# Optimization experiments

Hardware: AMD Instinct MI355X
Metric: run time of the kernel (lower is better)

The kernel has to match this reference:

```python
import jax, jax.numpy as jnp
import numpy as np

B, T, E, H = 4, 2048, 1024, 16
HS = E // H  # head_size = 64
FFN_HID = 100  # hard-coded in FeedForward
EPS = 1e-5


def layernorm(x, g, b):
    mu = jnp.mean(x, axis=-1, keepdims=True)
    var = jnp.mean(jnp.square(x - mu), axis=-1, keepdims=True)
    return (x - mu) * jax.lax.rsqrt(var + EPS) * g + b


def setup_inputs() -> dict:
    key = jax.random.key(0)
    ks = jax.random.split(key, 10)
    s = E ** -0.5
    return {
        "x": jax.random.normal(ks[0], (B, T, E), jnp.float32),
        "wq": jax.random.normal(ks[1], (E, E), jnp.float32) * s,
        "wk": jax.random.normal(ks[2], (E, E), jnp.float32) * s,
        "wv": jax.random.normal(ks[3], (E, E), jnp.float32) * s,
        "w_proj": jax.random.normal(ks[4], (E, E), jnp.float32) * s,
        "b_proj": jnp.zeros((E,), jnp.float32),
        "w1": jax.random.normal(ks[5], (E, FFN_HID), jnp.float32) * s,
        "b1": jnp.zeros((FFN_HID,), jnp.float32),
        "w2": jax.random.normal(ks[6], (FFN_HID, E), jnp.float32) * (FFN_HID ** -0.5),
        "b2": jnp.zeros((E,), jnp.float32),
        "ln1_g": jnp.ones((E,), jnp.float32),
        "ln1_b": jnp.zeros((E,), jnp.float32),
        "ln2_g": jnp.ones((E,), jnp.float32),
        "ln2_b": jnp.zeros((E,), jnp.float32),
    }


def reference(x, wq, wk, wv, w_proj, b_proj, w1, b1, w2, b2, ln1_g, ln1_b, ln2_g, ln2_b):
    # --- self-attention with pre-LN residual ---
    h = layernorm(x, ln1_g, ln1_b)  # [B,T,E]
    def split_heads(y):  # [B,T,E] -> [B,H,T,HS]
        return y.reshape(B, T, H, HS).transpose(0, 2, 1, 3)
    q = split_heads(h @ wq)
    k = split_heads(h @ wk)
    v = split_heads(h @ wv)
    # NOTE: original scales by C**-0.5 with C = n_embd (not head_size)
    wei = jnp.einsum("bhtd,bhsd->bhts", q, k) * (E ** -0.5)  # [B,H,T,T]
    causal = jnp.tril(jnp.ones((T, T), bool))
    wei = jnp.where(causal, wei, -jnp.inf)
    wei = jax.nn.softmax(wei, axis=-1)
    att = jnp.einsum("bhts,bhsd->bhtd", wei, v)  # [B,H,T,HS]
    att = att.transpose(0, 2, 1, 3).reshape(B, T, E)  # concat heads
    x = x + att @ w_proj + b_proj
    # --- feedforward with pre-LN residual ---
    h2 = layernorm(x, ln2_g, ln2_b)
    ff = jax.nn.relu(h2 @ w1 + b1) @ w2 + b2
    return x + ff
```

## Files before the change

### kernel.cpp

```cpp
#include <hip/hip_runtime.h>

typedef unsigned short u16;
typedef unsigned int u32;
typedef __bf16 bf16x8 __attribute__((ext_vector_type(8)));
typedef float f32x4 __attribute__((ext_vector_type(4)));

#define BDIM 4
#define TDIM 2048
#define EDIM 1024
#define HDIM 16
#define HS 64
#define MROWS (BDIM * TDIM)
#define FFNP 128

__device__ __forceinline__ u16 f2bf(float f) {
    __bf16 h = (__bf16)f;
    return __builtin_bit_cast(u16, h);
}

__device__ __forceinline__ void glds16(const void* g, void* l) {
    __builtin_amdgcn_global_load_lds(
        (__attribute__((address_space(1))) const void*)g,
        (__attribute__((address_space(3))) void*)l, 16, 0, 0);
}

__global__ __launch_bounds__(256) void transpose_all(
    const float* __restrict__ wq, const float* __restrict__ wk,
    const float* __restrict__ wv, const float* __restrict__ wproj,
    const float* __restrict__ w1, const float* __restrict__ w2,
    u16* __restrict__ wqkvt, u16* __restrict__ wpt,
    u16* __restrict__ w1t, u16* __restrict__ w2t)
{
    __shared__ u16 sm[64][72];
    const float* src; u16* dst;
    int K, N, Kpad, Npad;
    switch (blockIdx.z) {
        case 0: src = wq;    dst = wqkvt;                 K = N = Kpad = Npad = 1024; break;
        case 1: src = wk;    dst = wqkvt + 1024 * 1024;   K = N = Kpad = Npad = 1024; break;
        case 2: src = wv;    dst = wqkvt + 2 * 1024 * 1024; K = N = Kpad = Npad = 1024; break;
        case 3: src = wproj; dst = wpt;                   K = N = Kpad = Npad = 1024; break;
        case 4: src = w1;    dst = w1t; K = 1024; N = 100; Kpad = 1024; Npad = 128; break;
        default: src = w2;   dst = w2t; K = 100; N = 1024; Kpad = 128; Npad = 1024; break;
    }
    int k0 = blockIdx.x * 64, n0 = blockIdx.y * 64;
    if (k0 >= Kpad || n0 >= Npad) return;
    int tid = threadIdx.x;
#pragma unroll
    for (int i = 0; i < 16; i++) {
        int idx = i * 256 + tid;
        int kl = idx >> 6, nl = idx & 63;
        int k = k0 + kl, n = n0 + nl;
        float v = (k < K && n < N) ? src[(size_t)k * N + n] : 0.f;
        sm[kl][nl] = f2bf(v);
    }
    __syncthreads();
#pragma unroll
    for (int i = 0; i < 16; i++) {
        int idx = i * 256 + tid;
        int nl = idx >> 6, kl = idx & 63;
        int n = n0 + nl, k = k0 + kl;
        if (n < Npad && k < Kpad) dst[(size_t)n * Kpad + k] = sm[kl][nl];
    }
}

__global__ __launch_bounds__(256) void ln_rows(
    const float* __restrict__ X, const float* __restrict__ G,
    const float* __restrict__ Bv, u16* __restrict__ H)
{
    int w = threadIdx.x >> 6, l = threadIdx.x & 63;
    int row = blockIdx.x * 4 + w;
    const float* xr = X + (size_t)row * EDIM;
    float4 v[4];
    float s = 0.f, s2 = 0.f;
#pragma unroll
    for (int i = 0; i < 4; i++) {
        v[i] = *(const float4*)&xr[l * 4 + i * 256];
        s += v[i].x + v[i].y + v[i].z + v[i].w;
        s2 += v[i].x * v[i].x + v[i].y * v[i].y + v[i].z * v[i].z + v[i].w * v[i].w;
    }
#pragma unroll
    for (int off = 1; off < 64; off <<= 1) {
        s += __shfl_xor(s, off, 64);
        s2 += __shfl_xor(s2, off, 64);
    }
    float mean = s * (1.f / EDIM);
    float var = s2 * (1.f / EDIM) - mean * mean;
    float rstd = rsqrtf(var + 1e-5f);
#pragma unroll
    for (int i = 0; i < 4; i++) {
        int c = l * 4 + i * 256;
        float4 gg = *(const float4*)&G[c];
        float4 bb = *(const float4*)&Bv[c];
        u16 o0 = f2bf((v[i].x - mean) * rstd * gg.x + bb.x);
        u16 o1 = f2bf((v[i].y - mean) * rstd * gg.y + bb.y);
        u16 o2 = f2bf((v[i].z - mean) * rstd * gg.z + bb.z);
        u16 o3 = f2bf((v[i].w - mean) * rstd * gg.w + bb.w);
        uint2 pk;
        pk.x = (u32)o0 | ((u32)o1 << 16);
        pk.y = (u32)o2 | ((u32)o3 << 16);
        *(uint2*)&H[(size_t)row * EDIM + c] = pk;
    }
}

#define LDA4(d, mfb)                                                          \
    _Pragma("unroll") for (int mi = 0; mi < 4; mi++)                          \
    _Pragma("unroll") for (int ks = 0; ks < 2; ks++)                          \
        a[mi][ks] = *(const bf16x8*)&L[d][0][wm][((mfb + mi) * 16 + lr) * 64  \
                        + (((lg + 4 * ks) ^ (lr & 7)) << 3)];
#define LDB2(d, nfb)                                                          \
    _Pragma("unroll") for (int ni = 0; ni < 2; ni++)                          \
    _Pragma("unroll") for (int ks = 0; ks < 2; ks++)                          \
        b[ni][ks] = *(const bf16x8*)&L[d][1][wh][((wn & 1) * 64               \
                        + (nfb + ni) * 16 + lr) * 64                          \
                        + (((lg + 4 * ks) ^ (lr & 7)) << 3)];
#define MFMAQ(mfb, nfb)                                                       \
    _Pragma("unroll") for (int mi = 0; mi < 4; mi++)                          \
    _Pragma("unroll") for (int ni = 0; ni < 2; ni++)                          \
    _Pragma("unroll") for (int ks = 0; ks < 2; ks++)                          \
        acc[mfb + mi][nfb + ni] = __builtin_amdgcn_mfma_f32_16x16x32_bf16(    \
            a[mi][ks], b[ni][ks], acc[mfb + mi][nfb + ni], 0, 0, 0);
#define PH_SYNC1()                                                            \
    __builtin_amdgcn_s_barrier();                                             \
    asm volatile("s_waitcnt lgkmcnt(0)" ::: "memory");                        \
    __builtin_amdgcn_sched_barrier(0);                                        \
    __builtin_amdgcn_s_setprio(1);
#define PH_SYNC2()                                                            \
    __builtin_amdgcn_s_setprio(0);                                            \
    __builtin_amdgcn_s_barrier();
#define PH_SYNC2V(cond)                                                       \
    __builtin_amdgcn_s_setprio(0);                                            \
    if (cond) { asm volatile("s_waitcnt vmcnt(2)" ::: "memory"); }            \
    else      { asm volatile("s_waitcnt vmcnt(0)" ::: "memory"); }            \
    __builtin_amdgcn_s_barrier();

__global__ __launch_bounds__(512, 2) void gemm256_qkv(
    const u16* __restrict__ A, const u16* __restrict__ Bt,
    u16* __restrict__ Cb, u16* __restrict__ vtp)
{
    __shared__ u16 L[2][2][2][128 * 64];
    const u16 *pA, *pB;
    int bx, by;
    bool vmode = false;
    {
        int id = blockIdx.x;
        if (id < 256) {
            int sw = (id & 7) * 32 + (id >> 3);
            bx = sw % 32; by = sw / 32;
            pA = A; pB = Bt;
        } else {
            id -= 256;
            int sw = (id & 7) * 16 + (id >> 3);
            bx = sw % 4; by = sw / 4;
            pA = Bt + (size_t)2048 * 1024;
            pB = A;
            vmode = true;
        }
    }
    const int m0 = bx * 256, n0 = by * 256;

    const int tid = threadIdx.x;
    const int w = tid >> 6, l = tid & 63;
    const int wm = w >> 2, wn = w & 3, wh = wn >> 1;
    const int lg = l >> 4, lr = l & 15;

    const int srow = w * 16 + (l >> 3);
    const int sch8 = ((l & 7) ^ (l >> 3)) * 8;

    auto stA = [&](int d, int h, int t) {
        const u16* src = pA + (size_t)(m0 + h * 128 + srow) * 1024 + t * 64 + sch8;
        u16* dst = &L[d][0][h][w * 1024];
        glds16(src, dst);
        glds16(src + (size_t)8 * 1024, dst + 512);
    };
    auto stB = [&](int d, int h, int t) {
        const u16* src = pB + (size_t)(n0 + h * 128 + srow) * 1024 + t * 64 + sch8;
        u16* dst = &L[d][1][h][w * 1024];
        glds16(src, dst);
        glds16(src + (size_t)8 * 1024, dst + 512);
    };

    f32x4 acc[8][4];
#pragma unroll
    for (int i = 0; i < 8; i++)
#pragma unroll
        for (int j = 0; j < 4; j++) acc[i][j] = f32x4{0.f, 0.f, 0.f, 0.f};
    bf16x8 a[4][2], b[2][2];

    const int NI = 1024 >> 7;

    stA(0, 0, 0); stA(0, 1, 0); stB(0, 0, 0); stB(0, 1, 0);
    stB(1, 0, 1);
    asm volatile("s_waitcnt vmcnt(2)" ::: "memory");
    __builtin_amdgcn_s_barrier();

#pragma unroll 1
    for (int j = 0; j < NI; j++) {
        const int t = 2 * j;
        const bool more = (j + 1 < NI);
        LDA4(0, 0); LDB2(0, 0);
        stA(1, 0, t + 1);
        PH_SYNC1(); MFMAQ(0, 0); PH_SYNC2();
        LDA4(0, 4);
        stA(1, 1, t + 1);
        PH_SYNC1(); MFMAQ(4, 0); PH_SYNC2();
        LDB2(0, 2);
        stB(1, 1, t + 1);
        PH_SYNC1(); MFMAQ(4, 2); PH_SYNC2();
        LDA4(0, 0);
        if (more) stB(0, 1, t + 2);
        PH_SYNC1(); MFMAQ(0, 2); PH_SYNC2V(more);
        LDA4(1, 0); LDB2(1, 0);
        if (more) stA(0, 0, t + 2);
        PH_SYNC1(); MFMAQ(0, 0); PH_SYNC2();
        LDA4(1, 4);
        if (more) stA(0, 1, t + 2);
        PH_SYNC1(); MFMAQ(4, 0); PH_SYNC2();
        LDB2(1, 2);
        if (more) stB(0, 0, t + 2);
        PH_SYNC1(); MFMAQ(4, 2); PH_SYNC2();
        LDA4(1, 0);
        if (more) stB(1, 0, t + 3);
        PH_SYNC1(); MFMAQ(0, 2); PH_SYNC2V(more);
    }

#pragma unroll
    for (int mf = 0; mf < 8; mf++) {
#pragma unroll
        for (int nf = 0; nf < 4; nf++) {
#pragma unroll
            for (int e = 0; e < 4; e++) {
                int row = m0 + wm * 128 + mf * 16 + lg * 4 + e;
                int col = n0 + wn * 64 + nf * 16 + lr;
                float v = acc[mf][nf][e];
                if (!vmode) {
                    Cb[(size_t)row * 2048 + col] = f2bf(v);
                } else {
                    int bq = col >> 11, tt = col & 2047;
                    vtp[((size_t)bq * 1024 + row) * 2048 + tt] = f2bf(v);
                }
            }
        }
    }
}

template <int MODE>
__global__ __launch_bounds__(256, 2) void gemm_bt(
    const u16* __restrict__ A, const u16* __restrict__ Bt,
    float* __restrict__ Cf,
    const float* __restrict__ resid, const float* __restrict__ bias,
    int M, int N, int K, int lda, int ldb, int mb)
{
    __shared__ u16 As[2][128 * 32];
    __shared__ u16 Bs[2][128 * 32];
    int bx, by;
    if constexpr (MODE == 4) {
        bx = blockIdx.x; by = blockIdx.y;
        int kz = blockIdx.z;
        A += kz * 256;
        Bt += kz * 256;
        Cf += (size_t)kz * M * N;
    } else {
        int nwg = gridDim.x, id = blockIdx.x;
        int sw = (id & 7) * (nwg >> 3) + (id >> 3);
        bx = sw % mb; by = sw / mb;
    }
    const int tid = threadIdx.x;
    const int w = tid >> 6, l = tid & 63;
    const int wr = w >> 1, wc = w & 1;
    const int lg = l >> 4, lr = l & 15;
    const int m0 = bx * 128, n0 = by * 128;

    f32x4 zero = {0.f, 0.f, 0.f, 0.f};
    f32x4 acc[4][4];
#pragma unroll
    for (int i = 0; i < 4; i++)
#pragma unroll
        for (int j = 0; j < 4; j++) acc[i][j] = zero;

    const u16* Ag = A + (size_t)(m0 + w * 16 + (l >> 2)) * lda + (l & 3) * 8;
    const u16* Bg = Bt + (size_t)(n0 + w * 16 + (l >> 2)) * ldb + (l & 3) * 8;

    auto stage = [&](int b, int k0) {
        glds16(Ag + k0, &As[b][w * 512]);
        glds16(Ag + k0 + (size_t)64 * lda, &As[b][w * 512 + 2048]);
        glds16(Bg + k0, &Bs[b][w * 512]);
        glds16(Bg + k0 + (size_t)64 * ldb, &Bs[b][w * 512 + 2048]);
    };
    auto compute = [&](int b) {
        bf16x8 af[4], bfr[4];
#pragma unroll
        for (int t = 0; t < 4; t++)
            af[t] = *(const bf16x8*)&As[b][(wr * 64 + t * 16 + lr) * 32 + lg * 8];
#pragma unroll
        for (int t = 0; t < 4; t++)
            bfr[t] = *(const bf16x8*)&Bs[b][(wc * 64 + t * 16 + lr) * 32 + lg * 8];
#pragma unroll
        for (int i = 0; i < 4; i++)
#pragma unroll
            for (int j = 0; j < 4; j++)
                acc[i][j] = __builtin_amdgcn_mfma_f32_16x16x32_bf16(
                    af[i], bfr[j], acc[i][j], 0, 0, 0);
    };

    stage(0, 0);
    __syncthreads();
    int cur = 0;
    for (int k0 = 32; k0 < K; k0 += 32) {
        stage(cur ^ 1, k0);
        compute(cur);
        __syncthreads();
        cur ^= 1;
    }
    compute(cur);

#pragma unroll
    for (int i = 0; i < 4; i++) {
#pragma unroll
        for (int j = 0; j < 4; j++) {
#pragma unroll
            for (int e = 0; e < 4; e++) {
                int row = m0 + wr * 64 + i * 16 + lg * 4 + e;
                int col = n0 + wc * 64 + j * 16 + lr;
                float v = acc[i][j][e];
                size_t idx = (size_t)row * N + col;
                if constexpr (MODE == 1 || MODE == 3) {
                    Cf[idx] = resid[idx] + v + bias[col];
                } else {
                    Cf[idx] = v;
                }
            }
        }
    }
}

__global__ __launch_bounds__(256) void relu_reduce4(
    const float* __restrict__ fp, const float* __restrict__ b1,
    u16* __restrict__ tb)
{
    const size_t CH = (size_t)MROWS * FFNP;
    size_t base = ((size_t)blockIdx.x * 256 + threadIdx.x) * 4;
    float4 s0 = *(const float4*)&fp[base];
    float4 s1 = *(const float4*)&fp[base + CH];
    float4 s2 = *(const float4*)&fp[base + 2 * CH];
    float4 s3 = *(const float4*)&fp[base + 3 * CH];
    int col = (int)(base & (FFNP - 1));
    float sv[4] = {s0.x + s1.x + s2.x + s3.x, s0.y + s1.y + s2.y + s3.y,
                   s0.z + s1.z + s2.z + s3.z, s0.w + s1.w + s2.w + s3.w};
    u16 o[4];
#pragma unroll
    for (int j = 0; j < 4; j++) {
        int c = col + j;
        float b = (c < 100) ? b1[c] : 0.f;
        o[j] = f2bf(fmaxf(sv[j] + b, 0.f));
    }
    uint2 pk;
    pk.x = (u32)o[0] | ((u32)o[1] << 16);
    pk.y = (u32)o[2] | ((u32)o[3] << 16);
    *(uint2*)&tb[base] = pk;
}

__global__ __launch_bounds__(256, 4) void attn_fwd(
    const u16* __restrict__ qk, const u16* __restrict__ Vt,
    u16* __restrict__ Og)
{
    int xcd = blockIdx.x & 7;
    int j = blockIdx.x >> 3;
    int bh = xcd * 8 + (j & 7);
    int qp = j >> 3;
    int bb = bh >> 4, hh = bh & 15;

    int tid = threadIdx.x;
    int w = tid >> 6, l = tid & 63;
    int lg = l >> 4, lr = l & 15;

    const u16* Qb = qk + ((size_t)bb * TDIM) * 2048 + hh * HS;
    const u16* Kb = Qb + 1024;
    const u16* Vb = Vt + (size_t)bh * HS * TDIM;

    __shared__ u16 Ks[2][64 * 64];
    __shared__ u16 Vs[2][64 * 64];
    __shared__ u16 Ps[4][16 * 64];

    int srow = w * 16 + (l >> 3);
    int schunk = (l & 7) ^ ((l >> 3) & 7);
    u16* Pw = Ps[w];
    int sbase = (l & 48) + lg * 4;

    const float QSCL = 0.045084227f;

#pragma unroll 1
    for (int qi = 0; qi < 2; qi++) {
        int qb = (qi == 0 ? qp : 31 - qp) * 64;
        int q_abs = qb + w * 16 + lr;
        int wlo = qb + w * 16;
        int nt = qb / 64 + 1;

        bf16x8 qf[2];
        qf[0] = *(const bf16x8*)&Qb[(size_t)q_abs * 2048 + lg * 8];
        qf[1] = *(const bf16x8*)&Qb[(size_t)q_abs * 2048 + 32 + lg * 8];
#pragma unroll
        for (int i = 0; i < 8; i++) {
            qf[0][i] = (__bf16)((float)qf[0][i] * QSCL);
            qf[1][i] = (__bf16)((float)qf[1][i] * QSCL);
        }

        f32x4 zero = {0.f, 0.f, 0.f, 0.f};
        f32x4 oacc[4];
#pragma unroll
        for (int dt = 0; dt < 4; dt++) oacc[dt] = zero;
        float lpart = 0.f;

        auto stage = [&](int b, int kv0) {
            glds16(Kb + (size_t)(kv0 + srow) * 2048 + schunk * 8, &Ks[b][w * 1024]);
            glds16(Kb + (size_t)(kv0 + srow + 8) * 2048 + schunk * 8,
                   &Ks[b][w * 1024 + 512]);
            glds16(Vb + (size_t)srow * TDIM + kv0 + schunk * 8, &Vs[b][w * 1024]);
            glds16(Vb + (size_t)(srow + 8) * TDIM + kv0 + schunk * 8,
                   &Vs[b][w * 1024 + 512]);
        };

        stage(0, 0);
        if (nt > 1) stage(1, 64);
#pragma unroll 1
        for (int t = 0; t < nt; t++) {
            int kv0 = t * 64;
            int buf = t & 1;
            if (t + 1 < nt) { asm volatile("s_waitcnt vmcnt(4)" ::: "memory"); }
            else            { asm volatile("s_waitcnt vmcnt(0)" ::: "memory"); }
            __builtin_amdgcn_sched_barrier(0);
            __builtin_amdgcn_s_barrier();
            const u16* Kc = Ks[buf];
            const u16* Vc = Vs[buf];
            f32x4 sc[4];
#pragma unroll
            for (int ct = 0; ct < 4; ct++) sc[ct] = zero;
            __builtin_amdgcn_s_setprio(1);
#pragma unroll
            for (int ct = 0; ct < 4; ct++) {
#pragma unroll
                for (int dc = 0; dc < 2; dc++) {
                    bf16x8 kf = *(const bf16x8*)&Kc[(ct * 16 + lr) * 64 +
                                                    (((lg + 4 * dc) ^ (lr & 7)) << 3)];
                    sc[ct] = __builtin_amdgcn_mfma_f32_16x16x32_bf16(
                        kf, qf[dc], sc[ct], 0, 0, 0);
                }
            }
            __builtin_amdgcn_s_setprio(0);
            bf16x8 vfr[2][4];
#pragma unroll
            for (int m = 0; m < 2; m++)
#pragma unroll
                for (int dt = 0; dt < 4; dt++)
                    vfr[m][dt] = *(const bf16x8*)&Vc[(dt * 16 + lr) * 64 +
                                                     (((lg + 4 * m) ^ (lr & 7)) << 3)];
            float p[16];
            if (kv0 + 63 > wlo) {
#pragma unroll
                for (int ct = 0; ct < 4; ct++) {
#pragma unroll
                    for (int e = 0; e < 4; e++) {
                        float v = sc[ct][e];
                        if (kv0 + ct * 16 + lg * 4 + e > q_abs) v = -1e30f;
                        p[ct * 4 + e] = v;
                    }
                }
            } else {
#pragma unroll
                for (int ct = 0; ct < 4; ct++) {
#pragma unroll
                    for (int e = 0; e < 4; e++) p[ct * 4 + e] = sc[ct][e];
                }
            }
            float psum = 0.f;
#pragma unroll
            for (int i = 0; i < 16; i++) {
                p[i] = __builtin_amdgcn_exp2f(p[i]);
                psum += p[i];
            }
            lpart += psum;
#pragma unroll
            for (int ct = 0; ct < 4; ct++) {
#pragma unroll
                for (int i = 0; i < 2; i++) {
                    u32 word = (u32)f2bf(p[ct * 4 + 2 * i]) |
                               ((u32)f2bf(p[ct * 4 + 2 * i + 1]) << 16);
                    int kvb = ct * 16 + lg * 4 + 2 * i;
                    int idx = lr * 64 + ((((kvb >> 3) ^ (lr & 7)) << 3) | (kvb & 7));
                    *(u32*)&Pw[idx] = word;
                }
            }
            asm volatile("s_waitcnt lgkmcnt(0)" ::: "memory");
            __builtin_amdgcn_sched_barrier(0);
            __builtin_amdgcn_s_setprio(1);
#pragma unroll
            for (int m = 0; m < 2; m++) {
                bf16x8 pa = *(const bf16x8*)&Pw[lr * 64 + (((lg + 4 * m) ^ (lr & 7)) << 3)];
#pragma unroll
                for (int dt = 0; dt < 4; dt++) {
                    oacc[dt] = __builtin_amdgcn_mfma_f32_16x16x32_bf16(
                        pa, vfr[m][dt], oacc[dt], 0, 0, 0);
                }
            }
            __builtin_amdgcn_s_setprio(0);
            __builtin_amdgcn_s_barrier();
            if (t + 2 < nt) stage(buf, kv0 + 128);
        }
        float lsum = lpart;
        lsum += __shfl_xor(lsum, 16, 64);
        lsum += __shfl_xor(lsum, 32, 64);
        float lT[4];
#pragma unroll
        for (int e = 0; e < 4; e++) lT[e] = __shfl(lsum, sbase + e, 64);
#pragma unroll
        for (int dt = 0; dt < 4; dt++) {
#pragma unroll
            for (int e = 0; e < 4; e++) {
                int row = qb + w * 16 + lg * 4 + e;
                Og[((size_t)bb * TDIM + row) * EDIM + hh * HS + dt * 16 + lr] =
                    f2bf(oacc[dt][e] / lT[e]);
            }
        }
    }
}

extern "C" void kernel_launch(void* const* d_in, const int* in_sizes, int n_in,
                              void* d_out, int out_size, void* d_ws, size_t ws_size,
                              hipStream_t stream)
{
    const float* x     = (const float*)d_in[0];
    const float* wq    = (const float*)d_in[1];
    const float* wk    = (const float*)d_in[2];
    const float* wv    = (const float*)d_in[3];
    const float* wproj = (const float*)d_in[4];
    const float* bproj = (const float*)d_in[5];
    const float* w1    = (const float*)d_in[6];
    const float* b1    = (const float*)d_in[7];
    const float* w2    = (const float*)d_in[8];
    const float* b2    = (const float*)d_in[9];
    const float* ln1g  = (const float*)d_in[10];
    const float* ln1b  = (const float*)d_in[11];
    const float* ln2g  = (const float*)d_in[12];
    const float* ln2b  = (const float*)d_in[13];
    float* out = (float*)d_out;

    char* ws = (char*)d_ws;
    size_t off = 0;
    auto alloc = [&](size_t bytes) -> void* {
        void* p = (void*)(ws + off);
        off += (bytes + 255) & ~(size_t)255;
        return p;
    };
    u16* hbuf = (u16*)alloc((size_t)MROWS * EDIM * 2);
    u16* qk   = (u16*)alloc((size_t)MROWS * 2048 * 2);
    u16* attb = (u16*)alloc((size_t)MROWS * EDIM * 2);
    u16* vt   = (u16*)alloc((size_t)MROWS * EDIM * 2);
    u16* wqkvt = (u16*)alloc((size_t)3072 * EDIM * 2);
    u16* wpt  = (u16*)alloc((size_t)EDIM * EDIM * 2);
    u16* w1t  = (u16*)alloc((size_t)FFNP * EDIM * 2);
    u16* w2t  = (u16*)alloc((size_t)EDIM * FFNP * 2);
    float* fp = (float*)qk;
    u16* tb   = vt;

    transpose_all<<<dim3(16, 16, 6), 256, 0, stream>>>(
        wq, wk, wv, wproj, w1, w2, wqkvt, wpt, w1t, w2t);

    ln_rows<<<MROWS / 4, 256, 0, stream>>>(x, ln1g, ln1b, hbuf);
    gemm256_qkv<<<dim3(384), 512, 0, stream>>>(hbuf, wqkvt, qk, vt);
    attn_fwd<<<dim3(1024), 256, 0, stream>>>(qk, vt, attb);
    gemm_bt<1><<<dim3(512), 256, 0, stream>>>(attb, wpt, out, x, bproj,
                                              MROWS, EDIM, EDIM, EDIM, EDIM, 64);
    ln_rows<<<MROWS / 4, 256, 0, stream>>>(out, ln2g, ln2b, hbuf);
    gemm_bt<4><<<dim3(64, 1, 4), 256, 0, stream>>>(hbuf, w1t, fp, nullptr, nullptr,
                                                   MROWS, FFNP, 256, EDIM, EDIM, 64);
    relu_reduce4<<<dim3(MROWS * FFNP / 1024), 256, 0, stream>>>(fp, b1, tb);
    gemm_bt<3><<<dim3(512), 256, 0, stream>>>(tb, w2t, out, out, b2,
                                              MROWS, EDIM, FFNP, FFNP, FFNP, 64);
}
```

Measured before the change: 216.7 us.

## Split V projection out of fused QKV GEMM and vectorize P stores

The fused QKV GEMM previously handled the transposed V projection with extra blocks inside the same 256x256 kernel. Those 128 blocks moved into a separate launch of the generic 128-tile GEMM with a new mode that writes the transposed bf16 V output. The intent is to remove the mixed-role tail in the big kernel, at the cost of an extra launch and a less tuned GEMM path for V. The attention kernel also packs each P fragment into one 8-byte LDS store instead of two 4-byte stores, with Ps aligned to 16 bytes.

```diff
diff --git a/kernel.cpp b/kernel.cpp
--- a/kernel.cpp
+++ b/kernel.cpp
@@ -133,29 +133,14 @@
     else      { asm volatile("s_waitcnt vmcnt(0)" ::: "memory"); }            \
     __builtin_amdgcn_s_barrier();
 
-__global__ __launch_bounds__(512, 2) void gemm256_qkv(
+__global__ __launch_bounds__(512, 2) void gemm256_qk(
     const u16* __restrict__ A, const u16* __restrict__ Bt,
-    u16* __restrict__ Cb, u16* __restrict__ vtp)
+    u16* __restrict__ Cb)
 {
     __shared__ u16 L[2][2][2][128 * 64];
-    const u16 *pA, *pB;
-    int bx, by;
-    bool vmode = false;
-    {
-        int id = blockIdx.x;
-        if (id < 256) {
-            int sw = (id & 7) * 32 + (id >> 3);
-            bx = sw % 32; by = sw / 32;
-            pA = A; pB = Bt;
-        } else {
-            id -= 256;
-            int sw = (id & 7) * 16 + (id >> 3);
-            bx = sw % 4; by = sw / 4;
-            pA = Bt + (size_t)2048 * 1024;
-            pB = A;
-            vmode = true;
-        }
-    }
+    int id = blockIdx.x;
+    int sw = (id & 7) * 32 + (id >> 3);
+    int bx = sw % 32, by = sw / 32;
     const int m0 = bx * 256, n0 = by * 256;
 
     const int tid = threadIdx.x;
@@ -167,13 +152,13 @@
     const int sch8 = ((l & 7) ^ (l >> 3)) * 8;
 
     auto stA = [&](int d, int h, int t) {
-        const u16* src = pA + (size_t)(m0 + h * 128 + srow) * 1024 + t * 64 + sch8;
+        const u16* src = A + (size_t)(m0 + h * 128 + srow) * 1024 + t * 64 + sch8;
         u16* dst = &L[d][0][h][w * 1024];
         glds16(src, dst);
         glds16(src + (size_t)8 * 1024, dst + 512);
     };
     auto stB = [&](int d, int h, int t) {
-        const u16* src = pB + (size_t)(n0 + h * 128 + srow) * 1024 + t * 64 + sch8;
+        const u16* src = Bt + (size_t)(n0 + h * 128 + srow) * 1024 + t * 64 + sch8;
         u16* dst = &L[d][1][h][w * 1024];
         glds16(src, dst);
         glds16(src + (size_t)8 * 1024, dst + 512);
@@ -231,13 +216,7 @@
             for (int e = 0; e < 4; e++) {
                 int row = m0 + wm * 128 + mf * 16 + lg * 4 + e;
                 int col = n0 + wn * 64 + nf * 16 + lr;
-                float v = acc[mf][nf][e];
-                if (!vmode) {
-                    Cb[(size_t)row * 2048 + col] = f2bf(v);
-                } else {
-                    int bq = col >> 11, tt = col & 2047;
-                    vtp[((size_t)bq * 1024 + row) * 2048 + tt] = f2bf(v);
-                }
+                Cb[(size_t)row * 2048 + col] = f2bf(acc[mf][nf][e]);
             }
         }
     }
@@ -322,11 +301,15 @@
                 int row = m0 + wr * 64 + i * 16 + lg * 4 + e;
                 int col = n0 + wc * 64 + j * 16 + lr;
                 float v = acc[i][j][e];
-                size_t idx = (size_t)row * N + col;
                 if constexpr (MODE == 1 || MODE == 3) {
+                    size_t idx = (size_t)row * N + col;
                     Cf[idx] = resid[idx] + v + bias[col];
+                } else if constexpr (MODE == 4) {
+                    Cf[(size_t)row * N + col] = v;
                 } else {
-                    Cf[idx] = v;
+                    u16* vtp = (u16*)Cf;
+                    int bq = col >> 11, tt = col & 2047;
+                    vtp[((size_t)bq * 1024 + row) * 2048 + tt] = f2bf(v);
                 }
             }
         }
@@ -379,7 +362,7 @@
 
     __shared__ u16 Ks[2][64 * 64];
     __shared__ u16 Vs[2][64 * 64];
-    __shared__ u16 Ps[4][16 * 64];
+    __shared__ __align__(16) u16 Ps[4][16 * 64];
 
     int srow = w * 16 + (l >> 3);
     int schunk = (l & 7) ^ ((l >> 3) & 7);
@@ -480,14 +463,12 @@
             lpart += psum;
 #pragma unroll
             for (int ct = 0; ct < 4; ct++) {
-#pragma unroll
-                for (int i = 0; i < 2; i++) {
-                    u32 word = (u32)f2bf(p[ct * 4 + 2 * i]) |
-                               ((u32)f2bf(p[ct * 4 + 2 * i + 1]) << 16);
-                    int kvb = ct * 16 + lg * 4 + 2 * i;
-                    int idx = lr * 64 + ((((kvb >> 3) ^ (lr & 7)) << 3) | (kvb & 7));
-                    *(u32*)&Pw[idx] = word;
-                }
+                uint2 pr;
+                pr.x = (u32)f2bf(p[ct * 4 + 0]) | ((u32)f2bf(p[ct * 4 + 1]) << 16);
+                pr.y = (u32)f2bf(p[ct * 4 + 2]) | ((u32)f2bf(p[ct * 4 + 3]) << 16);
+                int kvb = ct * 16 + lg * 4;
+                int idx = lr * 64 + ((((kvb >> 3) ^ (lr & 7)) << 3) | (kvb & 7));
+                *(uint2*)&Pw[idx] = pr;
             }
             asm volatile("s_waitcnt lgkmcnt(0)" ::: "memory");
             __builtin_amdgcn_sched_barrier(0);
@@ -565,7 +546,10 @@
         wq, wk, wv, wproj, w1, w2, wqkvt, wpt, w1t, w2t);
 
     ln_rows<<<MROWS / 4, 256, 0, stream>>>(x, ln1g, ln1b, hbuf);
-    gemm256_qkv<<<dim3(384), 512, 0, stream>>>(hbuf, wqkvt, qk, vt);
+    gemm256_qk<<<dim3(256), 512, 0, stream>>>(hbuf, wqkvt, qk);
+    gemm_bt<5><<<dim3(512), 256, 0, stream>>>(wqkvt + (size_t)2048 * 1024, hbuf,
+                                              (float*)vt, nullptr, nullptr,
+                                              1024, 8192, 1024, 1024, 1024, 8);
     attn_fwd<<<dim3(1024), 256, 0, stream>>>(qk, vt, attb);
     gemm_bt<1><<<dim3(512), 256, 0, stream>>>(attb, wpt, out, x, bproj,
                                               MROWS, EDIM, EDIM, EDIM, EDIM, 64);
```

New measurement: 216.5 us. About the same (-0.1%).
